# Kernel optimization log

Hardware: AMD Instinct MI355X
Metric: run time of the kernel (lower is better)

## Reference

```python
import jax, jax.numpy as jnp
import numpy as np

N_NODES = 20000
N_EDGES = 320000
F_IN = 512
F_OUT = 1024
N_GRAPHS = 64


def gcn_conv(x, src, dst, ew, W, b, n_nodes):
    xw = x @ W  # [N, Fout]
    loop = jnp.arange(n_nodes)
    s = jnp.concatenate([src, loop])
    d = jnp.concatenate([dst, loop])
    w = jnp.concatenate([ew, jnp.ones((n_nodes,), dtype=x.dtype)])
    deg = jax.ops.segment_sum(w, d, num_segments=n_nodes)  # in-degree by weight
    dinv = jnp.where(deg > 0, jax.lax.rsqrt(deg), 0.0).astype(x.dtype)
    norm = dinv[s] * w * dinv[d]  # [E+N]
    msg = norm[:, None] * xw[s]  # [E+N, Fout]
    out = jax.ops.segment_sum(msg, d, num_segments=n_nodes)
    return out + b


def mean_pool(x, batch, n_graphs):
    sums = jax.ops.segment_sum(x, batch, num_segments=n_graphs)
    cnt = jax.ops.segment_sum(jnp.ones((x.shape[0],), dtype=x.dtype), batch, num_segments=n_graphs)
    return sums / jnp.maximum(cnt, 1.0)[:, None]


def setup_inputs() -> dict:
    key = jax.random.key(0)
    ks = jax.random.split(key, 8)
    node_features = jax.random.normal(ks[0], (N_NODES, F_IN), dtype=jnp.float32)
    edge_index = jax.random.randint(ks[1], (2, N_EDGES), 0, N_NODES, dtype=jnp.int64)
    edge_weight = jax.random.uniform(ks[2], (N_EDGES,), dtype=jnp.float32)
    batch = jnp.sort(jax.random.randint(ks[3], (N_NODES,), 0, N_GRAPHS, dtype=jnp.int64))
    # Glorot-style params for the two GCNConv layers
    W1 = jax.random.normal(ks[4], (F_IN, F_OUT), dtype=jnp.float32) / np.sqrt(F_IN)
    b1 = jnp.zeros((F_OUT,), dtype=jnp.float32)
    W2 = jax.random.normal(ks[5], (F_OUT, F_OUT), dtype=jnp.float32) / np.sqrt(F_OUT)
    b2 = jnp.zeros((F_OUT,), dtype=jnp.float32)
    return {"node_features": node_features, "edge_index": edge_index,
            "edge_weight": edge_weight, "batch": batch,
            "W1": W1, "b1": b1, "W2": W2, "b2": b2}


def reference(node_features, edge_index, edge_weight, batch, W1, b1, W2, b2):
    n_nodes = node_features.shape[0]
    src, dst = edge_index[0], edge_index[1]
    h = jax.nn.relu(gcn_conv(node_features, src, dst, edge_weight, W1, b1, n_nodes))
    h = jax.nn.relu(gcn_conv(h, src, dst, edge_weight, W2, b2, n_nodes))
    return mean_pool(h, batch, N_GRAPHS)  # [G, F_OUT]
```

## Files before the change

kernel.cpp:

```cpp
#include <hip/hip_runtime.h>

#define N_NODES 20000
#define N_PAD   20480
#define N_EDGES 320000
#define F_IN 512
#define F_OUT 1024
#define N_GRAPHS 64
#define ESTRIDE 64

typedef __attribute__((ext_vector_type(8))) short bf16x8;
typedef __attribute__((ext_vector_type(16))) float f32x16;
typedef __attribute__((ext_vector_type(8))) unsigned short ushort8v;

static __device__ __forceinline__ unsigned short f2bf(float f) {
    unsigned int u = __float_as_uint(f);
    u = (u + 0x7fff + ((u >> 16) & 1)) >> 16;
    return (unsigned short)u;
}
static __device__ __forceinline__ float bf2f(unsigned short s) {
    return __uint_as_float(((unsigned int)s) << 16);
}

__global__ void k_setup(float* deg, int* cursor, float* out,
                        const int* __restrict__ batch, int* gstart) {
    int i = blockIdx.x * 256 + threadIdx.x;
    if (i < N_NODES) { deg[i] = 1.0f; cursor[i] = 0; }
    if (i < N_GRAPHS * F_OUT) out[i] = 0.f;
    if (i <= N_GRAPHS) {
        if (i == N_GRAPHS) gstart[i] = N_NODES;
        else {
            int lo = 0, hi = N_NODES;
            while (lo < hi) {
                int mid = (lo + hi) >> 1;
                if (batch[mid] < i) lo = mid + 1; else hi = mid;
            }
            gstart[i] = lo;
        }
    }
}

#define NB_E    ((N_EDGES + 255) / 256)
#define NB_WT   ((F_OUT / 32) * (F_IN / 32 + F_OUT / 32))
#define NB_CX   (N_PAD * (F_IN / 8) / 256)
__global__ __launch_bounds__(256) void k_pre(const int* __restrict__ dst,
                                             const float* __restrict__ ew,
                                             float* deg,
                                             const float* __restrict__ W1,
                                             unsigned short* __restrict__ Wt1,
                                             const float* __restrict__ W2,
                                             unsigned short* __restrict__ Wt2,
                                             const float* __restrict__ x,
                                             unsigned short* __restrict__ xb) {
    __shared__ float tile[32][33];
    const int bid = blockIdx.x;
    if (bid < NB_E) {
        int e = bid * 256 + threadIdx.x;
        if (e < N_EDGES) atomicAdd(&deg[dst[e]], ew[e]);
    } else if (bid < NB_E + NB_WT) {
        int cid = bid - NB_E;
        int by = cid >> 5;
        int n0 = (cid & 31) * 32;
        const float* W; unsigned short* Wt; int K, k0;
        if (by < F_IN / 32) { W = W1; Wt = Wt1; K = F_IN;  k0 = by * 32; }
        else                { W = W2; Wt = Wt2; K = F_OUT; k0 = (by - F_IN / 32) * 32; }
        int tx = threadIdx.x & 31;
        int ty = threadIdx.x >> 5;
#pragma unroll
        for (int i = 0; i < 32; i += 8)
            tile[ty + i][tx] = W[(size_t)(k0 + ty + i) * F_OUT + n0 + tx];
        __syncthreads();
#pragma unroll
        for (int i = 0; i < 32; i += 8)
            Wt[(size_t)(n0 + ty + i) * K + k0 + tx] = f2bf(tile[tx][ty + i]);
    } else {
        int idx = (bid - NB_E - NB_WT) * 256 + threadIdx.x;
        int row = idx >> 6;
        int c8 = (idx & 63) * 8;
        if (row >= N_PAD) return;
        ushort8v v;
        if (row < N_NODES) {
            const float* p = &x[(size_t)row * F_IN + c8];
#pragma unroll
            for (int i = 0; i < 8; i++) v[i] = f2bf(p[i]);
        } else {
#pragma unroll
            for (int i = 0; i < 8; i++) v[i] = 0;
        }
        *(ushort8v*)&xb[(size_t)row * F_IN + c8] = v;
    }
}

__global__ void k_fill(const int* __restrict__ src, const int* __restrict__ dst,
                       const float* __restrict__ ew, const float* __restrict__ deg,
                       int* cursor, unsigned int* __restrict__ csre) {
    int e = blockIdx.x * 256 + threadIdx.x;
    if (e < N_EDGES) {
        int d = dst[e], s = src[e];
        int pos = atomicAdd(&cursor[d], 1);
        if (pos < ESTRIDE) {
            float w = rsqrtf(deg[s]) * ew[e] * rsqrtf(deg[d]);
            csre[d * ESTRIDE + pos] = ((unsigned int)f2bf(w) << 16) | (unsigned int)s;
        }
    }
}

__global__ __launch_bounds__(64) void k_aggr_slab(const unsigned short* __restrict__ xin,
                                                  const float* __restrict__ deg,
                                                  const int* __restrict__ cursor,
                                                  const unsigned int* __restrict__ csre,
                                                  const float* __restrict__ bias,
                                                  unsigned short* __restrict__ outp,
                                                  int F, int act) {
    const int bid = blockIdx.x;
    const int slab = bid & 7;
    const int ng = bid >> 3;
    const int lane = threadIdx.x;
    const int n = ng * 8 + (lane >> 3);
    const int c = blockIdx.y * 512 + slab * 64 + (lane & 7) * 8;

    if (n >= N_NODES) {
        ushort8v z;
#pragma unroll
        for (int i = 0; i < 8; i++) z[i] = 0;
        *(ushort8v*)&outp[(size_t)n * F + c] = z;
        return;
    }

    const float di = rsqrtf(deg[n]);
    const float wself = di * di;
    float a[8];
    {
        ushort8v v = *(const ushort8v*)&xin[(size_t)n * F + c];
#pragma unroll
        for (int i = 0; i < 8; i++) a[i] = bf2f(v[i]) * wself;
    }

    const unsigned int* ce = csre + (size_t)n * ESTRIDE;
    const int cnt = min(cursor[n], ESTRIDE);
    int j = 0;
    for (; j + 4 <= cnt; j += 4) {
        uint4 m = *(const uint4*)&ce[j];
        ushort8v u0 = *(const ushort8v*)&xin[(size_t)(m.x & 0xFFFF) * F + c];
        ushort8v u1 = *(const ushort8v*)&xin[(size_t)(m.y & 0xFFFF) * F + c];
        ushort8v u2 = *(const ushort8v*)&xin[(size_t)(m.z & 0xFFFF) * F + c];
        ushort8v u3 = *(const ushort8v*)&xin[(size_t)(m.w & 0xFFFF) * F + c];
        float w0 = bf2f((unsigned short)(m.x >> 16));
        float w1 = bf2f((unsigned short)(m.y >> 16));
        float w2 = bf2f((unsigned short)(m.z >> 16));
        float w3 = bf2f((unsigned short)(m.w >> 16));
#pragma unroll
        for (int i = 0; i < 8; i++) {
            a[i] += w0 * bf2f(u0[i]);
            a[i] += w1 * bf2f(u1[i]);
            a[i] += w2 * bf2f(u2[i]);
            a[i] += w3 * bf2f(u3[i]);
        }
    }
    for (; j < cnt; j++) {
        unsigned int m = ce[j];
        float w = bf2f((unsigned short)(m >> 16));
        ushort8v u = *(const ushort8v*)&xin[(size_t)(m & 0xFFFF) * F + c];
#pragma unroll
        for (int i = 0; i < 8; i++) a[i] += w * bf2f(u[i]);
    }

    ushort8v r;
    if (act) {
#pragma unroll
        for (int i = 0; i < 8; i++) r[i] = f2bf(fmaxf(a[i] + bias[c + i], 0.f));
    } else {
#pragma unroll
        for (int i = 0; i < 8; i++) r[i] = f2bf(a[i]);
    }
    *(ushort8v*)&outp[(size_t)n * F + c] = r;
}

__global__ __launch_bounds__(256) void k_gemm_bf16(const unsigned short* __restrict__ A,
                                                   const unsigned short* __restrict__ Bt,
                                                   unsigned short* __restrict__ C, int K,
                                                   const float* __restrict__ bias, int act) {
    __shared__ short As[128 * 64];
    __shared__ short Bs[128 * 64];
    const int bid = blockIdx.x;
    const int xcd = bid & 7;
    const int i2 = bid >> 3;
    const int colb = i2 & 7;
    const int rowb = xcd * 20 + (i2 >> 3);
    const int row0 = rowb * 128;
    const int col0 = colb * 128;

    const int tid = threadIdx.x;
    const int lane = tid & 63;
    const int wave = tid >> 6;
    const int wm = wave >> 1, wn = wave & 1;
    const int l5 = lane & 31;
    const int kh = lane >> 5;

    f32x16 acc[2][2] = {};

    for (int k0 = 0; k0 < K; k0 += 64) {
#pragma unroll
        for (int it = 0; it < 4; it++) {
            int idx = it * 256 + tid;
            int r = idx >> 3;
            int g = (idx & 7) ^ (r & 7);
            const unsigned short* ga = &A[(size_t)(row0 + r) * K + k0 + g * 8];
            __builtin_amdgcn_global_load_lds(
                (const __attribute__((address_space(1))) void*)ga,
                (__attribute__((address_space(3))) void*)&As[idx * 8], 16, 0, 0);
            const unsigned short* gb = &Bt[(size_t)(col0 + r) * K + k0 + g * 8];
            __builtin_amdgcn_global_load_lds(
                (const __attribute__((address_space(1))) void*)gb,
                (__attribute__((address_space(3))) void*)&Bs[idx * 8], 16, 0, 0);
        }
        __syncthreads();

#pragma unroll
        for (int kk = 0; kk < 4; kk++) {
            const int g = kk * 2 + kh;
            bf16x8 af[2], bfr[2];
#pragma unroll
            for (int i = 0; i < 2; i++) {
                int ar = wm * 64 + i * 32 + l5;
                af[i] = *(const bf16x8*)&As[(ar * 8 + (g ^ (ar & 7))) * 8];
            }
#pragma unroll
            for (int j = 0; j < 2; j++) {
                int br = wn * 64 + j * 32 + l5;
                bfr[j] = *(const bf16x8*)&Bs[(br * 8 + (g ^ (br & 7))) * 8];
            }
#pragma unroll
            for (int i = 0; i < 2; i++)
#pragma unroll
                for (int j = 0; j < 2; j++)
                    acc[i][j] = __builtin_amdgcn_mfma_f32_32x32x16_bf16(
                        af[i], bfr[j], acc[i][j], 0, 0, 0);
        }
        __syncthreads();
    }

#pragma unroll
    for (int i = 0; i < 2; i++) {
#pragma unroll
        for (int j = 0; j < 2; j++) {
            int rbase = row0 + wm * 64 + i * 32 + kh * 4;
            int c = col0 + wn * 64 + j * 32 + l5;
            float bv = act ? bias[c] : 0.f;
#pragma unroll
            for (int reg = 0; reg < 16; reg++) {
                int rrow = rbase + (reg & 3) + 8 * (reg >> 2);
                float v = acc[i][j][reg];
                if (act) v = fmaxf(v + bv, 0.f);
                C[(size_t)rrow * F_OUT + c] = f2bf(v);
            }
        }
    }
}

__global__ __launch_bounds__(256) void k_pool(const unsigned short* __restrict__ h,
                                              const int* __restrict__ batch,
                                              const int* __restrict__ gstart,
                                              float* __restrict__ out) {
    const int r0 = blockIdx.x * 64;
    const int rowsub = threadIdx.x >> 7;
    const int c = (threadIdx.x & 127) * 8;
    const int rend = min(r0 + 64, N_NODES);
    int row = r0 + rowsub;
    if (row >= rend) return;

    float a[8] = {};
    int gcur = batch[row];
    for (; row < rend; row += 2) {
        int g = batch[row];
        if (g != gcur) {
            float inv = 1.0f / (float)max(gstart[gcur + 1] - gstart[gcur], 1);
#pragma unroll
            for (int i = 0; i < 8; i++) {
                atomicAdd(&out[(size_t)gcur * F_OUT + c + i], a[i] * inv);
                a[i] = 0.f;
            }
            gcur = g;
        }
        ushort8v v = *(const ushort8v*)&h[(size_t)row * F_OUT + c];
#pragma unroll
        for (int i = 0; i < 8; i++) a[i] += bf2f(v[i]);
    }
    float inv = 1.0f / (float)max(gstart[gcur + 1] - gstart[gcur], 1);
#pragma unroll
    for (int i = 0; i < 8; i++)
        atomicAdd(&out[(size_t)gcur * F_OUT + c + i], a[i] * inv);
}

extern "C" void kernel_launch(void* const* d_in, const int* in_sizes, int n_in,
                              void* d_out, int out_size, void* d_ws, size_t ws_size,
                              hipStream_t stream) {
    const float* x    = (const float*)d_in[0];
    const int* ei     = (const int*)d_in[1];
    const float* ew   = (const float*)d_in[2];
    const int* batch  = (const int*)d_in[3];
    const float* W1   = (const float*)d_in[4];
    const float* b1   = (const float*)d_in[5];
    const float* W2   = (const float*)d_in[6];
    const float* b2   = (const float*)d_in[7];
    float* out = (float*)d_out;

    const int* src = ei;
    const int* dst = ei + N_EDGES;

    char* ws = (char*)d_ws;
    const size_t SZ_XB  = (size_t)N_PAD * F_IN * 2;
    const size_t SZ_AX  = (size_t)N_PAD * F_IN * 2;
    const size_t SZ_WT1 = (size_t)F_OUT * F_IN * 2;
    const size_t SZ_WT2 = (size_t)F_OUT * F_OUT * 2;
    const size_t SZ_B   = (size_t)N_PAD * F_OUT * 2;
    unsigned short* xb  = (unsigned short*)(ws);
    unsigned short* ax  = (unsigned short*)(ws + SZ_XB);
    unsigned short* Wt1 = (unsigned short*)(ws + SZ_XB + SZ_AX);
    unsigned short* Wt2 = (unsigned short*)(ws + SZ_XB + SZ_AX + SZ_WT1);
    unsigned short* h1  = (unsigned short*)(ws + SZ_XB + SZ_AX + SZ_WT1 + SZ_WT2);
    unsigned short* xw2 = (unsigned short*)(ws + SZ_XB + SZ_AX + SZ_WT1 + SZ_WT2 + SZ_B);
    unsigned short* h2  = (unsigned short*)(ws);
    size_t off = SZ_XB + SZ_AX + SZ_WT1 + SZ_WT2 + 2 * SZ_B;
    auto alloc = [&](size_t bytes) -> void* {
        void* p = ws + off;
        off += (bytes + 255) & ~(size_t)255;
        return p;
    };
    float*        deg    = (float*)       alloc((size_t)N_NODES * 4);
    int*          cursor = (int*)         alloc((size_t)N_NODES * 4);
    unsigned int* csre   = (unsigned int*)alloc((size_t)N_NODES * ESTRIDE * 4);
    int*          gstart = (int*)         alloc((size_t)(N_GRAPHS + 1) * 4);

    k_setup<<<(N_GRAPHS * F_OUT + 255) / 256, 256, 0, stream>>>(deg, cursor, out, batch, gstart);
    k_pre<<<NB_E + NB_WT + NB_CX, 256, 0, stream>>>(dst, ew, deg, W1, Wt1, W2, Wt2, x, xb);
    k_fill<<<NB_E, 256, 0, stream>>>(src, dst, ew, deg, cursor, csre);
    k_aggr_slab<<<dim3((N_PAD / 8) * 8, 1), 64, 0, stream>>>(xb, deg, cursor, csre,
                                                             (const float*)nullptr, ax, F_IN, 0);
    const int gemm_blocks = (N_PAD / 128) * (F_OUT / 128);
    k_gemm_bf16<<<gemm_blocks, 256, 0, stream>>>(ax, Wt1, h1, F_IN, b1, 1);
    k_gemm_bf16<<<gemm_blocks, 256, 0, stream>>>(h1, Wt2, xw2, F_OUT, (const float*)nullptr, 0);
    k_aggr_slab<<<dim3((N_PAD / 8) * 8, 2), 64, 0, stream>>>(xw2, deg, cursor, csre, b2, h2, F_OUT, 1);
    k_pool<<<(N_NODES + 63) / 64, 256, 0, stream>>>(h2, batch, gstart, out);
}
```

Measured before the change: 335.6 us.

## Replace GEMM with 3-stage LDS ring pipeline and 128x256 tiles

```diff
diff --git a/kernel.cpp b/kernel.cpp
--- a/kernel.cpp
+++ b/kernel.cpp
@@ -9,7 +9,7 @@
 #define ESTRIDE 64
 
 typedef __attribute__((ext_vector_type(8))) short bf16x8;
-typedef __attribute__((ext_vector_type(16))) float f32x16;
+typedef __attribute__((ext_vector_type(4))) float f32x4;
 typedef __attribute__((ext_vector_type(8))) unsigned short ushort8v;
 
 static __device__ __forceinline__ unsigned short f2bf(float f) {
@@ -175,83 +175,114 @@
     *(ushort8v*)&outp[(size_t)n * F + c] = r;
 }
 
-__global__ __launch_bounds__(256) void k_gemm_bf16(const unsigned short* __restrict__ A,
-                                                   const unsigned short* __restrict__ Bt,
-                                                   unsigned short* __restrict__ C, int K,
-                                                   const float* __restrict__ bias, int act) {
-    __shared__ short As[128 * 64];
-    __shared__ short Bs[128 * 64];
+__global__ __launch_bounds__(512) void k_gemm_ring3(const unsigned short* __restrict__ A,
+                                                    const unsigned short* __restrict__ Bt,
+                                                    unsigned short* __restrict__ C, int K,
+                                                    const float* __restrict__ bias, int act) {
+    __shared__ short As[3][128 * 64];
+    __shared__ short Bs[3][256 * 64];
+
     const int bid = blockIdx.x;
     const int xcd = bid & 7;
     const int i2 = bid >> 3;
-    const int colb = i2 & 7;
-    const int rowb = xcd * 20 + (i2 >> 3);
+    const int colb = i2 & 3;
+    const int rowb = xcd * 20 + (i2 >> 2);
     const int row0 = rowb * 128;
-    const int col0 = colb * 128;
+    const int col0 = colb * 256;
 
     const int tid = threadIdx.x;
     const int lane = tid & 63;
     const int wave = tid >> 6;
-    const int wm = wave >> 1, wn = wave & 1;
-    const int l5 = lane & 31;
-    const int kh = lane >> 5;
-
-    f32x16 acc[2][2] = {};
-
-    for (int k0 = 0; k0 < K; k0 += 64) {
+    const int wm = wave >> 2;
+    const int wn = wave & 3;
+    const int l16 = lane & 15;
+    const int kq = lane >> 4;
+
+    const int NT = K >> 6;
+
+    f32x4 acc[4][4] = {};
+
+    auto stage = [&](int t, int s) {
+        const int k0 = t * 64;
+#pragma unroll
+        for (int it = 0; it < 2; it++) {
+            int q = it * 512 + tid;
+            int r = q >> 3;
+            int g = (q & 7) ^ (r & 7);
+            __builtin_amdgcn_global_load_lds(
+                (const __attribute__((address_space(1))) void*)&A[(size_t)(row0 + r) * K + k0 + g * 8],
+                (__attribute__((address_space(3))) void*)&As[s][q * 8], 16, 0, 0);
+        }
 #pragma unroll
         for (int it = 0; it < 4; it++) {
-            int idx = it * 256 + tid;
-            int r = idx >> 3;
-            int g = (idx & 7) ^ (r & 7);
-            const unsigned short* ga = &A[(size_t)(row0 + r) * K + k0 + g * 8];
+            int q = it * 512 + tid;
+            int r = q >> 3;
+            int g = (q & 7) ^ (r & 7);
             __builtin_amdgcn_global_load_lds(
-                (const __attribute__((address_space(1))) void*)ga,
-                (__attribute__((address_space(3))) void*)&As[idx * 8], 16, 0, 0);
-            const unsigned short* gb = &Bt[(size_t)(col0 + r) * K + k0 + g * 8];
-            __builtin_amdgcn_global_load_lds(
-                (const __attribute__((address_space(1))) void*)gb,
-                (__attribute__((address_space(3))) void*)&Bs[idx * 8], 16, 0, 0);
-        }
-        __syncthreads();
-
-#pragma unroll
-        for (int kk = 0; kk < 4; kk++) {
-            const int g = kk * 2 + kh;
-            bf16x8 af[2], bfr[2];
-#pragma unroll
-            for (int i = 0; i < 2; i++) {
-                int ar = wm * 64 + i * 32 + l5;
-                af[i] = *(const bf16x8*)&As[(ar * 8 + (g ^ (ar & 7))) * 8];
-            }
-#pragma unroll
-            for (int j = 0; j < 2; j++) {
-                int br = wn * 64 + j * 32 + l5;
-                bfr[j] = *(const bf16x8*)&Bs[(br * 8 + (g ^ (br & 7))) * 8];
-            }
-#pragma unroll
-            for (int i = 0; i < 2; i++)
-#pragma unroll
-                for (int j = 0; j < 2; j++)
-                    acc[i][j] = __builtin_amdgcn_mfma_f32_32x32x16_bf16(
-                        af[i], bfr[j], acc[i][j], 0, 0, 0);
-        }
-        __syncthreads();
-    }
-
-#pragma unroll
-    for (int i = 0; i < 2; i++) {
-#pragma unroll
-        for (int j = 0; j < 2; j++) {
-            int rbase = row0 + wm * 64 + i * 32 + kh * 4;
-            int c = col0 + wn * 64 + j * 32 + l5;
-            float bv = act ? bias[c] : 0.f;
-#pragma unroll
-            for (int reg = 0; reg < 16; reg++) {
-                int rrow = rbase + (reg & 3) + 8 * (reg >> 2);
-                float v = acc[i][j][reg];
+                (const __attribute__((address_space(1))) void*)&Bt[(size_t)(col0 + r) * K + k0 + g * 8],
+                (__attribute__((address_space(3))) void*)&Bs[s][q * 8], 16, 0, 0);
+        }
+    };
+
+    stage(0, 0);
+    stage(1, 1);
+    asm volatile("s_waitcnt vmcnt(6)" ::: "memory");
+    __builtin_amdgcn_s_barrier();
+    __builtin_amdgcn_sched_barrier(0);
+
+    int s = 0;
+    for (int t = 0; t < NT; ++t) {
+        int s2 = s + 2; if (s2 >= 3) s2 -= 3;
+        if (t + 2 < NT) stage(t + 2, s2);
+
+        const short* Asl = As[s];
+        const short* Bsl = Bs[s];
+#pragma unroll
+        for (int ks = 0; ks < 2; ks++) {
+            bf16x8 af[4], bfr[4];
+#pragma unroll
+            for (int fr = 0; fr < 4; fr++) {
+                int r = wm * 64 + fr * 16 + l16;
+                int g = (ks * 4 + kq) ^ (r & 7);
+                af[fr] = *(const bf16x8*)&Asl[r * 64 + g * 8];
+            }
+#pragma unroll
+            for (int fc = 0; fc < 4; fc++) {
+                int r = wn * 64 + fc * 16 + l16;
+                int g = (ks * 4 + kq) ^ (r & 7);
+                bfr[fc] = *(const bf16x8*)&Bsl[r * 64 + g * 8];
+            }
+            __builtin_amdgcn_s_setprio(1);
+#pragma unroll
+            for (int fr = 0; fr < 4; fr++)
+#pragma unroll
+                for (int fc = 0; fc < 4; fc++)
+                    acc[fr][fc] = __builtin_amdgcn_mfma_f32_16x16x32_bf16(
+                        af[fr], bfr[fc], acc[fr][fc], 0, 0, 0);
+            __builtin_amdgcn_s_setprio(0);
+        }
+
+        if (t < NT - 1) {
+            if (t + 2 < NT) asm volatile("s_waitcnt vmcnt(6)" ::: "memory");
+            else            asm volatile("s_waitcnt vmcnt(0)" ::: "memory");
+            __builtin_amdgcn_s_barrier();
+            __builtin_amdgcn_sched_barrier(0);
+        }
+        s = s + 1; if (s >= 3) s -= 3;
+    }
+
+#pragma unroll
+    for (int fr = 0; fr < 4; fr++) {
+        int m0 = row0 + wm * 64 + fr * 16 + kq * 4;
+#pragma unroll
+        for (int fc = 0; fc < 4; fc++) {
+            int n = col0 + wn * 64 + fc * 16 + l16;
+            float bv = act ? bias[n] : 0.f;
+#pragma unroll
+            for (int reg = 0; reg < 4; reg++) {
+                float v = acc[fr][fc][reg];
                 if (act) v = fmaxf(v + bv, 0.f);
-                C[(size_t)rrow * F_OUT + c] = f2bf(v);
+                C[(size_t)(m0 + reg) * F_OUT + n] = f2bf(v);
             }
         }
     }
@@ -336,9 +367,9 @@
     k_fill<<<NB_E, 256, 0, stream>>>(src, dst, ew, deg, cursor, csre);
     k_aggr_slab<<<dim3((N_PAD / 8) * 8, 1), 64, 0, stream>>>(xb, deg, cursor, csre,
                                                              (const float*)nullptr, ax, F_IN, 0);
-    const int gemm_blocks = (N_PAD / 128) * (F_OUT / 128);
-    k_gemm_bf16<<<gemm_blocks, 256, 0, stream>>>(ax, Wt1, h1, F_IN, b1, 1);
-    k_gemm_bf16<<<gemm_blocks, 256, 0, stream>>>(h1, Wt2, xw2, F_OUT, (const float*)nullptr, 0);
+    const int gemm_blocks = (N_PAD / 128) * (F_OUT / 256);
+    k_gemm_ring3<<<gemm_blocks, 512, 0, stream>>>(ax, Wt1, h1, F_IN, b1, 1);
+    k_gemm_ring3<<<gemm_blocks, 512, 0, stream>>>(h1, Wt2, xw2, F_OUT, (const float*)nullptr, 0);
     k_aggr_slab<<<dim3((N_PAD / 8) * 8, 2), 64, 0, stream>>>(xw2, deg, cursor, csre, b2, h2, F_OUT, 1);
     k_pool<<<(N_NODES + 63) / 64, 256, 0, stream>>>(h2, batch, gstart, out);
 }
```

Result: slower. 375.0 us (+11.7%).
